# Performance work log

Measured on AMD Instinct MI355X. Metric: run time of the kernel, lower is better.

## Reference

```python
import jax, jax.numpy as jnp
import numpy as np

SDIM, EDIM, HID, DEPTH = 128, 128, 64, 4
CUTOFF, EPS = 5.0, 1e-6
N, E = 40000, 512000
MSG_IN = 2 * SDIM + EDIM + 2   # [s_src, s_dst, e, dist, ea_d]
SCAL_IN = SDIM + HID


def silu(x):
    return x * jax.nn.sigmoid(x)


def setup_inputs() -> dict:
    key = jax.random.key(0)
    ks = jax.random.split(key, 16)

    def w(k, shape, fan):
        return jax.random.normal(k, shape, jnp.float32) / np.float32(np.sqrt(fan))

    return {
        "s": jax.random.normal(ks[0], (N, SDIM), jnp.float32),
        "v": jax.random.normal(ks[1], (N, 3), jnp.float32),
        "e": jax.random.normal(ks[2], (E, EDIM), jnp.float32),
        "edge_index": jax.random.randint(ks[3], (2, E), 0, N),
        "ea_d": jax.random.uniform(ks[4], (E, 1), dtype=jnp.float32),
        "ea_r": jax.random.normal(ks[5], (E, 3), jnp.float32),
        "batch": jnp.zeros((N,), jnp.int32),
        "We1": w(ks[6], (DEPTH, MSG_IN, HID), MSG_IN),
        "be1": jnp.zeros((DEPTH, HID), jnp.float32),
        "We2": w(ks[7], (DEPTH, HID, HID), HID),
        "be2": jnp.zeros((DEPTH, HID), jnp.float32),
        "Weo": w(ks[8], (DEPTH, HID, EDIM), HID),
        "beo": jnp.zeros((DEPTH, EDIM), jnp.float32),
        "Wv": w(ks[9], (DEPTH, HID, 1), HID),
        "bv": jnp.zeros((DEPTH, 1), jnp.float32),
        "Ws1": w(ks[10], (DEPTH, SCAL_IN, HID), SCAL_IN),
        "bs1": jnp.zeros((DEPTH, HID), jnp.float32),
        "Ws2": w(ks[11], (DEPTH, HID, SDIM), HID),
        "bs2": jnp.zeros((DEPTH, SDIM), jnp.float32),
    }


def egnn_forward(s, v, e, src, dst, ea_d,
                 We1, be1, We2, be2, Weo, beo, Wv, bv, Ws1, bs1, Ws2, bs2):
    n = s.shape[0]
    ne = e.shape[0]
    # mean aggregation: per-destination degree (clamped to 1)
    deg = jax.ops.segment_sum(jnp.ones((ne, 1), s.dtype), dst, num_segments=n)
    deg = jnp.maximum(deg, 1.0)
    for i in range(DEPTH):
        rel = v[src] - v[dst]                                          # [E,3]
        dist = jnp.sqrt(jnp.sum(rel * rel, axis=-1, keepdims=True) + EPS)  # [E,1]
        cw = 0.5 * (jnp.cos(jnp.pi * dist / CUTOFF) + 1.0) * (dist < CUTOFF)
        h = jnp.concatenate([s[src], s[dst], e, dist, ea_d], axis=-1)  # [E,MSG_IN]
        m = silu(silu(h @ We1[i] + be1[i]) @ We2[i] + be2[i]) * cw      # [E,HID]
        e = e + m @ Weo[i] + beo[i]                                    # edge residual
        wv = m @ Wv[i] + bv[i]                                         # [E,1]
        v = v + jax.ops.segment_sum(rel * wv, dst, num_segments=n) / deg
        agg = jax.ops.segment_sum(m, dst, num_segments=n) / deg        # [N,HID]
        s = s + silu(jnp.concatenate([s, agg], axis=-1) @ Ws1[i] + bs1[i]) @ Ws2[i] + bs2[i]
    return s, v, e


def reference(s, v, e, edge_index, ea_d, ea_r, batch,
              We1, be1, We2, be2, Weo, beo, Wv, bv, Ws1, bs1, Ws2, bs2):
    del batch, ea_r  # unused in the enhanced (EGCL_Edge_Fast) path
    src, dst = edge_index[0], edge_index[1]
    return egnn_forward(s, v, e, src, dst, ea_d,
                        We1, be1, We2, be2, Weo, beo, Wv, bv, Ws1, bs1, Ws2, bs2)
```

## Files before the change

### kernel.cpp

```cpp
#include <hip/hip_runtime.h>
#include <math.h>

#define N_NODES 40000
#define N_EDGES 512000
#define SDIM 128
#define EDIM 128
#define HID 64
#define DEPTH 4
#define MSG_IN 386
#define SCAL_IN 192
#define CUTOFF 5.0f
#define EPS_D 1e-6f

#define TILE_M 16
#define EW 8
#define ETHREADS 512
#define EBLOCKS 256
#define TWAVES (EBLOCKS * EW)
#define NTILES (N_EDGES / TILE_M)
#define ATILES (N_NODES / TILE_M)
#define SCAN_B 1024
#define SCAN_NB ((N_NODES + SCAN_B - 1) / SCAN_B)

typedef __attribute__((ext_vector_type(8))) short short8;
typedef __attribute__((ext_vector_type(4))) float f32x4;
typedef unsigned long long ull;

__device__ __forceinline__ float silu_f(float x) { return x / (1.0f + __expf(-x)); }

__device__ __forceinline__ unsigned short f2b(float x) {
  union { __bf16 b; unsigned short u; } v;
  v.b = (__bf16)x;
  return v.u;
}

__device__ __forceinline__ float b2f(unsigned short u) {
  union { unsigned int u32; float f; } v; v.u32 = (unsigned int)u << 16; return v.f;
}

__device__ __forceinline__ short8 pack8(f32x4 lo, f32x4 hi) {
  union { unsigned short u[8]; short8 s; } pk;
  pk.u[0] = f2b(lo[0]); pk.u[1] = f2b(lo[1]); pk.u[2] = f2b(lo[2]); pk.u[3] = f2b(lo[3]);
  pk.u[4] = f2b(hi[0]); pk.u[5] = f2b(hi[1]); pk.u[6] = f2b(hi[2]); pk.u[7] = f2b(hi[3]);
  return pk.s;
}

__global__ __launch_bounds__(256) void k_zero(float* __restrict__ p, int n) {
  int i = blockIdx.x * 256 + threadIdx.x;
  int stride = gridDim.x * 256;
  for (; i < n; i += stride) p[i] = 0.0f;
}

__global__ __launch_bounds__(256) void k_cnt(const int* __restrict__ dst,
                                             int* __restrict__ cnt, int ne) {
  int i = blockIdx.x * 256 + threadIdx.x;
  if (i < ne) atomicAdd(&cnt[dst[i]], 1);
}

__global__ __launch_bounds__(256) void k_deginv_cnt(const int* __restrict__ cnt,
                                                    float* __restrict__ deginv, int n) {
  int i = blockIdx.x * 256 + threadIdx.x;
  if (i < n) deginv[i] = 1.0f / fmaxf((float)cnt[i], 1.0f);
}

__global__ __launch_bounds__(256) void k_scan1(const int* __restrict__ cnt,
                                               int* __restrict__ bstart,
                                               int* __restrict__ bsum, int n) {
  __shared__ int tmp[SCAN_B];
  const int base = blockIdx.x * SCAN_B;
  const int tid = threadIdx.x;
  for (int i = tid; i < SCAN_B; i += 256)
    tmp[i] = (base + i < n) ? cnt[base + i] : 0;
  __syncthreads();
  for (int off = 1; off < SCAN_B; off <<= 1) {
    int vals[4];
#pragma unroll
    for (int j = 0; j < 4; ++j) {
      const int i = tid + j * 256;
      vals[j] = (i >= off) ? tmp[i - off] : 0;
    }
    __syncthreads();
#pragma unroll
    for (int j = 0; j < 4; ++j) tmp[tid + j * 256] += vals[j];
    __syncthreads();
  }
  for (int i = tid; i < SCAN_B; i += 256)
    if (base + i < n) bstart[base + i] = tmp[i] - cnt[base + i];
  if (tid == 0) bsum[blockIdx.x] = tmp[SCAN_B - 1];
}

__global__ void k_scan2(int* __restrict__ bsum, int nb) {
  if (threadIdx.x == 0) {
    int run = 0;
    for (int i = 0; i < nb; ++i) { const int v = bsum[i]; bsum[i] = run; run += v; }
  }
}

__global__ __launch_bounds__(256) void k_scan3(int* __restrict__ bstart,
                                               const int* __restrict__ bsum,
                                               int* __restrict__ cursor, int n) {
  int i = blockIdx.x * 256 + threadIdx.x;
  if (i < n) {
    const int v = bstart[i] + bsum[i >> 10];
    bstart[i] = v;
    cursor[i] = v;
  }
}

__global__ __launch_bounds__(256) void k_scatter(const int* __restrict__ srcs,
                                                 const int* __restrict__ dsts,
                                                 const float* __restrict__ ead,
                                                 int* __restrict__ cursor,
                                                 int4* __restrict__ meta, int ne) {
  int i = blockIdx.x * 256 + threadIdx.x;
  if (i < ne) {
    const int d = dsts[i];
    const int pos = atomicAdd(&cursor[d], 1);
    int4 m;
    m.x = i; m.y = srcs[i]; m.z = d; m.w = __float_as_int(ead[i]);
    meta[pos] = m;
  }
}

__global__ __launch_bounds__(256) void k_prep(const int4* __restrict__ meta,
                                              const float* __restrict__ vbuf,
                                              float4* __restrict__ dynA,
                                              float* __restrict__ dynB, int ne) {
  int i = blockIdx.x * 256 + threadIdx.x;
  if (i < ne) {
    const int4 m = meta[i];
    const float dx = vbuf[m.y * 3 + 0] - vbuf[m.z * 3 + 0];
    const float dy = vbuf[m.y * 3 + 1] - vbuf[m.z * 3 + 1];
    const float dz = vbuf[m.y * 3 + 2] - vbuf[m.z * 3 + 2];
    const float dist = sqrtf(dx * dx + dy * dy + dz * dz + EPS_D);
    const float cwv = (dist < CUTOFF)
                          ? 0.5f * (__cosf((float)M_PI / CUTOFF * dist) + 1.0f)
                          : 0.0f;
    dynA[i] = make_float4(dx, dy, dz, dist);
    dynB[i] = cwv;
  }
}

__global__ __launch_bounds__(512, 2) void k_nodeA(
    const float* __restrict__ s, const float* __restrict__ W1,
    const float* __restrict__ be1_,
    unsigned short* __restrict__ SaP, unsigned short* __restrict__ SbP) {
  __shared__ __align__(16) unsigned short W1abt[64 * 264];
  __shared__ __align__(16) unsigned short snS[EW][16 * 136];
  const int tid = threadIdx.x, lane = tid & 63, w = tid >> 6;
  const int c = lane & 15, g = lane >> 4;
  for (int idx = tid; idx < 256 * 64; idx += 512) {
    const int k = idx >> 6, n = idx & 63;
    W1abt[n * 264 + k] = f2b(W1[idx]);
  }
  __syncthreads();
  float be1_l[4];
#pragma unroll
  for (int nt = 0; nt < 4; ++nt) be1_l[nt] = be1_[nt * 16 + c];
  unsigned short* sn = snS[w];

  for (int t = blockIdx.x * EW + w; t < ATILES; t += gridDim.x * EW) {
    const int n0 = t * TILE_M;
    const f32x4* sbase = (const f32x4*)(s + (size_t)n0 * SDIM);
#pragma unroll
    for (int i = 0; i < 4; ++i) {
      const int f = i * 128 + lane * 2;
      const f32x4 a = sbase[f], b = sbase[f + 1];
      *(short8*)&sn[(i * 4 + g) * 136 + c * 8] = pack8(a, b);
    }
    f32x4 aA[4], aB[4];
#pragma unroll
    for (int nt = 0; nt < 4; ++nt) {
      aA[nt] = f32x4{be1_l[nt], be1_l[nt], be1_l[nt], be1_l[nt]};
      aB[nt] = f32x4{0.f, 0.f, 0.f, 0.f};
    }
#pragma unroll
    for (int kc = 0; kc < 4; ++kc) {
      const short8 af = *(const short8*)&sn[c * 136 + kc * 32 + g * 8];
#pragma unroll
      for (int nt = 0; nt < 4; ++nt) {
        const short8 bfA = *(const short8*)&W1abt[(nt * 16 + c) * 264 + kc * 32 + g * 8];
        const short8 bfB = *(const short8*)&W1abt[(nt * 16 + c) * 264 + 128 + kc * 32 + g * 8];
        aA[nt] = __builtin_amdgcn_mfma_f32_16x16x32_bf16(af, bfA, aA[nt], 0, 0, 0);
        aB[nt] = __builtin_amdgcn_mfma_f32_16x16x32_bf16(af, bfB, aB[nt], 0, 0, 0);
      }
    }
#pragma unroll
    for (int r = 0; r < 4; ++r) {
      const size_t row = (size_t)(n0 + g * 4 + r);
      const ull pa = (ull)f2b(aA[0][r]) | ((ull)f2b(aA[1][r]) << 16)
                   | ((ull)f2b(aA[2][r]) << 32) | ((ull)f2b(aA[3][r]) << 48);
      const ull pb = (ull)f2b(aB[0][r]) | ((ull)f2b(aB[1][r]) << 16)
                   | ((ull)f2b(aB[2][r]) << 32) | ((ull)f2b(aB[3][r]) << 48);
      *(ull*)&SaP[row * 64 + c * 4] = pa;
      *(ull*)&SbP[row * 64 + c * 4] = pb;
    }
  }
}

__global__ __launch_bounds__(512, 2) void k_nodeC(
    const float* __restrict__ scur, float* __restrict__ s_dst,
    const float* __restrict__ vcur, float* __restrict__ v_dst,
    float* __restrict__ v_acc, float* __restrict__ agg,
    const float* __restrict__ deginv,
    const float* __restrict__ Ws1_, const float* __restrict__ bs1_,
    const float* __restrict__ Ws2_, const float* __restrict__ bs2_,
    const float* __restrict__ W1n, const float* __restrict__ be1n,
    unsigned short* __restrict__ SaP, unsigned short* __restrict__ SbP,
    int doA) {
  __shared__ __align__(16) unsigned short Ws1t[64 * 200];
  __shared__ __align__(16) unsigned short Ws2t[128 * 72];
  __shared__ __align__(16) unsigned short W1abt[64 * 264];
  __shared__ __align__(16) unsigned short sAS[EW][16 * 200];
  __shared__ __align__(16) unsigned short hS[EW][16 * 72];
  __shared__ float dS[EW][16];
  const int tid = threadIdx.x, lane = tid & 63, w = tid >> 6;
  const int c = lane & 15, g = lane >> 4;
  for (int idx = tid; idx < 192 * 64; idx += 512) {
    const int k = idx >> 6, n = idx & 63;
    Ws1t[n * 200 + k] = f2b(Ws1_[idx]);
  }
  for (int idx = tid; idx < 64 * 128; idx += 512) {
    const int k = idx >> 7, n = idx & 127;
    Ws2t[n * 72 + k] = f2b(Ws2_[idx]);
  }
  if (doA) {
    for (int idx = tid; idx < 256 * 64; idx += 512) {
      const int k = idx >> 6, n = idx & 63;
      W1abt[n * 264 + k] = f2b(W1n[idx]);
    }
  }
  __syncthreads();
  float bs1_l[4], bs2_l[8], be1_l[4];
#pragma unroll
  for (int nt = 0; nt < 4; ++nt) bs1_l[nt] = bs1_[nt * 16 + c];
#pragma unroll
  for (int j = 0; j < 8; ++j) bs2_l[j] = bs2_[j * 16 + c];
#pragma unroll
  for (int nt = 0; nt < 4; ++nt) be1_l[nt] = doA ? be1n[nt * 16 + c] : 0.0f;
  unsigned short* sA = sAS[w];
  unsigned short* hw = hS[w];

  for (int t = blockIdx.x * EW + w; t < ATILES; t += gridDim.x * EW) {
    const int n0 = t * TILE_M;
    if (lane < 16) dS[w][lane] = deginv[n0 + lane];
    if (lane < 48) {
      const int i3 = n0 * 3 + lane;
      v_dst[i3] = vcur[i3] + v_acc[i3] * dS[w][lane / 3];
      v_acc[i3] = 0.0f;
    }
    const f32x4* sbase = (const f32x4*)(scur + (size_t)n0 * SDIM);
#pragma unroll
    for (int i = 0; i < 4; ++i) {
      const int f = i * 128 + lane * 2;
      const f32x4 a = sbase[f], b = sbase[f + 1];
      *(short8*)&sA[(i * 4 + g) * 200 + c * 8] = pack8(a, b);
    }
#pragma unroll
    for (int i = 0; i < 4; ++i) {
      const int row = i * 4 + g;
      float* ab = agg + (size_t)(n0 + row) * HID + c * 4;
      const f32x4 av = *(const f32x4*)ab;
      const float di = dS[w][row];
      union { unsigned short u[4]; ull ll; } pk4;
      pk4.u[0] = f2b(av[0] * di); pk4.u[1] = f2b(av[1] * di);
      pk4.u[2] = f2b(av[2] * di); pk4.u[3] = f2b(av[3] * di);
      *(ull*)&sA[row * 200 + 128 + c * 4] = pk4.ll;
      *(f32x4*)ab = f32x4{0.f, 0.f, 0.f, 0.f};
    }
    f32x4 acc[4];
#pragma unroll
    for (int nt = 0; nt < 4; ++nt)
      acc[nt] = f32x4{bs1_l[nt], bs1_l[nt], bs1_l[nt], bs1_l[nt]};
#pragma unroll
    for (int kc = 0; kc < 6; ++kc) {
      const short8 af = *(const short8*)&sA[c * 200 + kc * 32 + g * 8];
#pragma unroll
      for (int nt = 0; nt < 4; ++nt) {
        const short8 bf = *(const short8*)&Ws1t[(nt * 16 + c) * 200 + kc * 32 + g * 8];
        acc[nt] = __builtin_amdgcn_mfma_f32_16x16x32_bf16(af, bf, acc[nt], 0, 0, 0);
      }
    }
#pragma unroll
    for (int nt = 0; nt < 4; ++nt)
#pragma unroll
      for (int r = 0; r < 4; ++r)
        hw[(g * 4 + r) * 72 + nt * 16 + c] = f2b(silu_f(acc[nt][r]));
    f32x4 o[8];
#pragma unroll
    for (int nt = 0; nt < 8; ++nt) o[nt] = f32x4{0.f, 0.f, 0.f, 0.f};
#pragma unroll
    for (int kc = 0; kc < 2; ++kc) {
      const short8 am = *(const short8*)&hw[c * 72 + kc * 32 + g * 8];
#pragma unroll
      for (int nt = 0; nt < 8; ++nt) {
        const short8 bf = *(const short8*)&Ws2t[(nt * 16 + c) * 72 + kc * 32 + g * 8];
        o[nt] = __builtin_amdgcn_mfma_f32_16x16x32_bf16(am, bf, o[nt], 0, 0, 0);
      }
    }
#pragma unroll
    for (int j = 0; j < 8; ++j) {
      const int col = j * 16 + c;
#pragma unroll
      for (int r = 0; r < 4; ++r) {
        const int row = g * 4 + r;
        const size_t gi = (size_t)(n0 + row) * SDIM + col;
        const float sum = o[j][r] + bs2_l[j] + scur[gi];
        s_dst[gi] = sum;
        if (doA) sA[row * 200 + col] = f2b(sum);
      }
    }
    if (doA) {
      f32x4 aA[4], aB[4];
#pragma unroll
      for (int nt = 0; nt < 4; ++nt) {
        aA[nt] = f32x4{be1_l[nt], be1_l[nt], be1_l[nt], be1_l[nt]};
        aB[nt] = f32x4{0.f, 0.f, 0.f, 0.f};
      }
#pragma unroll
      for (int kc = 0; kc < 4; ++kc) {
        const short8 af = *(const short8*)&sA[c * 200 + kc * 32 + g * 8];
#pragma unroll
        for (int nt = 0; nt < 4; ++nt) {
          const short8 bfA = *(const short8*)&W1abt[(nt * 16 + c) * 264 + kc * 32 + g * 8];
          const short8 bfB = *(const short8*)&W1abt[(nt * 16 + c) * 264 + 128 + kc * 32 + g * 8];
          aA[nt] = __builtin_amdgcn_mfma_f32_16x16x32_bf16(af, bfA, aA[nt], 0, 0, 0);
          aB[nt] = __builtin_amdgcn_mfma_f32_16x16x32_bf16(af, bfB, aB[nt], 0, 0, 0);
        }
      }
#pragma unroll
      for (int r = 0; r < 4; ++r) {
        const size_t row = (size_t)(n0 + g * 4 + r);
        const ull pa = (ull)f2b(aA[0][r]) | ((ull)f2b(aA[1][r]) << 16)
                     | ((ull)f2b(aA[2][r]) << 32) | ((ull)f2b(aA[3][r]) << 48);
        const ull pb = (ull)f2b(aB[0][r]) | ((ull)f2b(aB[1][r]) << 16)
                     | ((ull)f2b(aB[2][r]) << 32) | ((ull)f2b(aB[3][r]) << 48);
        *(ull*)&SaP[row * 64 + c * 4] = pa;
        *(ull*)&SbP[row * 64 + c * 4] = pb;
      }
    }
  }
}

template <typename TI, typename TO>
__global__ __launch_bounds__(ETHREADS, 1) void k_edge_mfma(
    const TI* __restrict__ e_src, TO* __restrict__ e_dst,
    const unsigned short* __restrict__ SaP, const unsigned short* __restrict__ SbP,
    const int4* __restrict__ meta, const float4* __restrict__ dynA,
    const float* __restrict__ dynB,
    const float* __restrict__ W1e,
    const float* __restrict__ w1d, const float* __restrict__ w1a,
    const float* __restrict__ We2_, const float* __restrict__ be2_,
    const float* __restrict__ Weo_, const float* __restrict__ beo_,
    const float* __restrict__ Wv_, const float* __restrict__ bv_,
    float* __restrict__ v_acc, float* __restrict__ agg) {
  constexpr bool IN16 = (sizeof(TI) == 2);
  constexpr bool OUT16 = (sizeof(TO) == 2);
  __shared__ __align__(16) unsigned short W1t[64 * 136];
  __shared__ __align__(16) unsigned short We2t[64 * 72];
  __shared__ __align__(16) unsigned short WeoT[128 * 72];
  __shared__ __align__(16) unsigned short eT[EW][TILE_M * 136];
  __shared__ __align__(16) float hm[EW][TILE_M * 68];
  __shared__ __align__(16) float sbufS[EW][2][160];

  const int tid = threadIdx.x;
  const int lane = tid & 63;
  const int w = tid >> 6;
  const int c = lane & 15;
  const int g = lane >> 4;

  for (int idx = tid; idx < 128 * 64; idx += ETHREADS) {
    const int k = idx >> 6, n = idx & 63;
    W1t[n * 136 + k] = f2b(W1e[idx]);
  }
  for (int idx = tid; idx < 64 * 64; idx += ETHREADS) {
    const int k = idx >> 6, n = idx & 63;
    We2t[n * 72 + k] = f2b(We2_[idx]);
  }
  for (int idx = tid; idx < 64 * 128; idx += ETHREADS) {
    const int k = idx >> 7, n = idx & 127;
    WeoT[n * 72 + k] = f2b(Weo_[idx]);
  }
  __syncthreads();

  float w1d_l[4], w1a_l[4], be2_l[4], Wv_l[4], beo_l[8];
#pragma unroll
  for (int nt = 0; nt < 4; ++nt) {
    w1d_l[nt] = w1d[nt * 16 + c];
    w1a_l[nt] = w1a[nt * 16 + c];
    be2_l[nt] = be2_[nt * 16 + c];
    Wv_l[nt]  = Wv_[nt * 16 + c];
  }
#pragma unroll
  for (int nt = 0; nt < 8; ++nt) beo_l[nt] = beo_[nt * 16 + c];
  const float bv0 = bv_[0];

  unsigned short* eTw = eT[w];
  float* hmw = hm[w];

  f32x4 eAf[8];
  short8 eAb[4];
  ull sabA[4], sabB[4];
  int4 metaR = {0, 0, 0, 0};
  float4 dynAR = {0.f, 0.f, 0.f, 0.f};
  float cwR = 0.f;

  const int t0 = blockIdx.x * EW + w;
  int cur = 0;

  {
    float* sb0 = &sbufS[w][0][0];
    int* sbi0 = (int*)sb0;
    if (lane < 16) {
      const int pos = t0 * TILE_M + lane;
      const int4 m = meta[pos];
      const float4 da = dynA[pos];
      const float cwv = dynB[pos];
      sb0[lane] = da.w; sb0[16 + lane] = cwv; sb0[32 + lane] = __int_as_float(m.w);
      sb0[48 + lane] = da.x; sb0[64 + lane] = da.y; sb0[80 + lane] = da.z;
      sbi0[96 + lane] = m.y; sbi0[112 + lane] = m.z; sbi0[128 + lane] = m.x;
    }
    if constexpr (IN16) {
      const int erc = sbi0[128 + c];
      const TI* rowp = e_src + (size_t)erc * EDIM;
#pragma unroll
      for (int kc = 0; kc < 4; ++kc)
        eAb[kc] = *(const short8*)(rowp + kc * 32 + g * 8);
    } else {
#pragma unroll
      for (int i = 0; i < 4; ++i) {
        const int er = sbi0[128 + i * 4 + g];
        const f32x4* eb = (const f32x4*)(e_src + (size_t)er * EDIM);
        eAf[i * 2] = eb[c * 2];
        eAf[i * 2 + 1] = eb[c * 2 + 1];
      }
    }
#pragma unroll
    for (int r = 0; r < 4; ++r) {
      sabA[r] = *(const ull*)&SaP[(size_t)sbi0[96 + g * 4 + r] * 64 + c * 4];
      sabB[r] = *(const ull*)&SbP[(size_t)sbi0[112 + g * 4 + r] * 64 + c * 4];
    }
    if (t0 + TWAVES < NTILES && lane < 16) {
      const int pos = (t0 + TWAVES) * TILE_M + lane;
      metaR = meta[pos]; dynAR = dynA[pos]; cwR = dynB[pos];
    }
  }

  for (int t = t0; t < NTILES; t += TWAVES) {
    const bool hasNext = (t + TWAVES) < NTILES;
    float* sbC = &sbufS[w][cur][0];
    int* sbiC = (int*)sbC;
    float* sbN = &sbufS[w][cur ^ 1][0];
    int* sbiN = (int*)sbN;

    if (hasNext && lane < 16) {
      sbN[lane] = dynAR.w; sbN[16 + lane] = cwR; sbN[32 + lane] = __int_as_float(metaR.w);
      sbN[48 + lane] = dynAR.x; sbN[64 + lane] = dynAR.y; sbN[80 + lane] = dynAR.z;
      sbiN[96 + lane] = metaR.y; sbiN[112 + lane] = metaR.z; sbiN[128 + lane] = metaR.x;
    }

    short8 afT[4];
    if constexpr (IN16) {
#pragma unroll
      for (int kc = 0; kc < 4; ++kc) afT[kc] = eAb[kc];
    } else {
#pragma unroll
      for (int i = 0; i < 4; ++i)
        *(short8*)&eT[w][(i * 4 + g) * 136 + c * 8] = pack8(eAf[i * 2], eAf[i * 2 + 1]);
    }

    float dist_r[4], cw_r[4], ea_r[4];
#pragma unroll
    for (int r = 0; r < 4; ++r) {
      const int row = g * 4 + r;
      dist_r[r] = sbC[row]; cw_r[r] = sbC[16 + row]; ea_r[r] = sbC[32 + row];
    }
    f32x4 acc[4];
#pragma unroll
    for (int nt = 0; nt < 4; ++nt)
#pragma unroll
      for (int r = 0; r < 4; ++r)
        acc[nt][r] = b2f((unsigned short)(sabA[r] >> (nt * 16)))
                   + b2f((unsigned short)(sabB[r] >> (nt * 16)))
                   + dist_r[r] * w1d_l[nt] + ea_r[r] * w1a_l[nt];

    if (hasNext) {
      if constexpr (IN16) {
        const int erc = sbiN[128 + c];
        const TI* rowp = e_src + (size_t)erc * EDIM;
#pragma unroll
        for (int kc = 0; kc < 4; ++kc)
          eAb[kc] = *(const short8*)(rowp + kc * 32 + g * 8);
      } else {
#pragma unroll
        for (int i = 0; i < 4; ++i) {
          const int er = sbiN[128 + i * 4 + g];
          const f32x4* eb = (const f32x4*)(e_src + (size_t)er * EDIM);
          eAf[i * 2] = eb[c * 2];
          eAf[i * 2 + 1] = eb[c * 2 + 1];
        }
      }
#pragma unroll
      for (int r = 0; r < 4; ++r) {
        sabA[r] = *(const ull*)&SaP[(size_t)sbiN[96 + g * 4 + r] * 64 + c * 4];
        sabB[r] = *(const ull*)&SbP[(size_t)sbiN[112 + g * 4 + r] * 64 + c * 4];
      }
      if (t + 2 * TWAVES < NTILES && lane < 16) {
        const int pos = (t + 2 * TWAVES) * TILE_M + lane;
        metaR = meta[pos]; dynAR = dynA[pos]; cwR = dynB[pos];
      }
    }

#pragma unroll
    for (int kc = 0; kc < 4; ++kc) {
      short8 af;
      if constexpr (IN16)
        af = afT[kc];
      else
        af = *(const short8*)&eTw[c * 136 + kc * 32 + g * 8];
#pragma unroll
      for (int nt = 0; nt < 4; ++nt) {
        const short8 bf = *(const short8*)&W1t[(nt * 16 + c) * 136 + kc * 32 + g * 8];
        acc[nt] = __builtin_amdgcn_mfma_f32_16x16x32_bf16(af, bf, acc[nt], 0, 0, 0);
      }
    }
#pragma unroll
    for (int nt = 0; nt < 4; ++nt)
#pragma unroll
      for (int r = 0; r < 4; ++r)
        hmw[(g * 4 + r) * 68 + nt * 16 + c] = silu_f(acc[nt][r]);

    f32x4 acc2[4];
#pragma unroll
    for (int nt = 0; nt < 4; ++nt)
      acc2[nt] = f32x4{be2_l[nt], be2_l[nt], be2_l[nt], be2_l[nt]};
#pragma unroll
    for (int kc = 0; kc < 2; ++kc) {
      const f32x4 lo = *(const f32x4*)&hmw[c * 68 + kc * 32 + g * 8];
      const f32x4 hi = *(const f32x4*)&hmw[c * 68 + kc * 32 + g * 8 + 4];
      const short8 am = pack8(lo, hi);
#pragma unroll
      for (int nt = 0; nt < 4; ++nt) {
        const short8 bf = *(const short8*)&We2t[(nt * 16 + c) * 72 + kc * 32 + g * 8];
        acc2[nt] = __builtin_amdgcn_mfma_f32_16x16x32_bf16(am, bf, acc2[nt], 0, 0, 0);
      }
    }
    float mval[4][4];
#pragma unroll
    for (int nt = 0; nt < 4; ++nt)
#pragma unroll
      for (int r = 0; r < 4; ++r)
        mval[nt][r] = silu_f(acc2[nt][r]) * cw_r[r];

#pragma unroll
    for (int nt = 0; nt < 4; ++nt)
#pragma unroll
      for (int r = 0; r < 4; ++r)
        hmw[(g * 4 + r) * 68 + nt * 16 + c] = mval[nt][r];

#pragma unroll
    for (int r = 0; r < 4; ++r) {
      float s = mval[0][r] * Wv_l[0];
#pragma unroll
      for (int nt = 1; nt < 4; ++nt) s = fmaf(mval[nt][r], Wv_l[nt], s);
      s += __shfl_xor(s, 1); s += __shfl_xor(s, 2);
      s += __shfl_xor(s, 4); s += __shfl_xor(s, 8);
      if (c == 0) sbC[144 + g * 4 + r] = s + bv0;
    }

    {
      float accum = 0.f;
#pragma unroll
      for (int row = 0; row < 16; ++row) {
        accum += hmw[row * 68 + lane];
        const int dd = sbiC[112 + row];
        const bool cut = (row == 15) || (sbiC[113 + row] != dd);
        if (cut) {
          atomicAdd(&agg[(size_t)dd * HID + lane], accum);
          accum = 0.f;
        }
      }
    }
    if (lane < 3) {
      float accum = 0.f;
#pragma unroll
      for (int row = 0; row < 16; ++row) {
        accum = fmaf(sbC[48 + 16 * lane + row], sbC[144 + row], accum);
        const int dd = sbiC[112 + row];
        const bool cut = (row == 15) || (sbiC[113 + row] != dd);
        if (cut) {
          atomicAdd(&v_acc[(size_t)dd * 3 + lane], accum);
          accum = 0.f;
        }
      }
    }

    f32x4 oacc[8];
#pragma unroll
    for (int nt = 0; nt < 8; ++nt)
      oacc[nt] = f32x4{beo_l[nt], beo_l[nt], beo_l[nt], beo_l[nt]};
#pragma unroll
    for (int kc = 0; kc < 2; ++kc) {
      const f32x4 lo = *(const f32x4*)&hmw[c * 68 + kc * 32 + g * 8];
      const f32x4 hi = *(const f32x4*)&hmw[c * 68 + kc * 32 + g * 8 + 4];
      const short8 am = pack8(lo, hi);
#pragma unroll
      for (int nt = 0; nt < 8; ++nt) {
        const short8 bf = *(const short8*)&WeoT[(nt * 16 + c) * 72 + kc * 32 + g * 8];
        oacc[nt] = __builtin_amdgcn_mfma_f32_16x16x32_bf16(am, bf, oacc[nt], 0, 0, 0);
      }
    }

#pragma unroll
    for (int h2 = 0; h2 < 2; ++h2) {
#pragma unroll
      for (int nt = 0; nt < 4; ++nt)
#pragma unroll
        for (int r = 0; r < 4; ++r)
          hmw[(g * 4 + r) * 68 + nt * 16 + c] = oacc[h2 * 4 + nt][r];
#pragma unroll
      for (int q = 0; q < 4; ++q) {
        const int row = q * 4 + g;
        const int er = sbiC[128 + row];
        const f32x4 val = *(const f32x4*)&hmw[row * 68 + c * 4];
        f32x4 old;
        if constexpr (IN16) {
          const ull ov = *(const ull*)&e_src[(size_t)er * EDIM + h2 * 64 + c * 4];
#pragma unroll
          for (int j = 0; j < 4; ++j)
            old[j] = b2f((unsigned short)(ov >> (16 * j)));
        } else {
          old = *(const f32x4*)&e_src[(size_t)er * EDIM + h2 * 64 + c * 4];
        }
        const f32x4 sum = val + old;
        if constexpr (OUT16) {
          union { unsigned short u[4]; ull ll; } pk4;
          pk4.u[0] = f2b(sum[0]); pk4.u[1] = f2b(sum[1]);
          pk4.u[2] = f2b(sum[2]); pk4.u[3] = f2b(sum[3]);
          *(ull*)&e_dst[(size_t)er * EDIM + h2 * 64 + c * 4] = pk4.ll;
        } else {
          *(f32x4*)&e_dst[(size_t)er * EDIM + h2 * 64 + c * 4] = sum;
        }
      }
    }
    cur ^= 1;
  }
}

extern "C" void kernel_launch(void* const* d_in, const int* in_sizes, int n_in,
                              void* d_out, int out_size, void* d_ws, size_t ws_size,
                              hipStream_t stream) {
  const float* s_in = (const float*)d_in[0];
  const float* v_in = (const float*)d_in[1];
  const float* e_in = (const float*)d_in[2];
  const int*   eidx = (const int*)d_in[3];
  const float* ead  = (const float*)d_in[4];
  const float* We1 = (const float*)d_in[7];
  const float* be1 = (const float*)d_in[8];
  const float* We2 = (const float*)d_in[9];
  const float* be2 = (const float*)d_in[10];
  const float* Weo = (const float*)d_in[11];
  const float* beo = (const float*)d_in[12];
  const float* Wv  = (const float*)d_in[13];
  const float* bv  = (const float*)d_in[14];
  const float* Ws1 = (const float*)d_in[15];
  const float* bs1 = (const float*)d_in[16];
  const float* Ws2 = (const float*)d_in[17];
  const float* bs2 = (const float*)d_in[18];

  float* out_s = (float*)d_out;
  float* out_v = out_s + (size_t)N_NODES * SDIM;
  float* out_e = out_v + (size_t)N_NODES * 3;

  float* ws     = (float*)d_ws;
  float* deginv = ws;
  float* v_acc  = deginv + N_NODES;
  float* agg    = v_acc + (size_t)3 * N_NODES;
  unsigned short* SaP = (unsigned short*)(agg + (size_t)64 * N_NODES);
  unsigned short* SbP = SaP + (size_t)64 * N_NODES;
  int* cnt     = (int*)(SbP + (size_t)64 * N_NODES);
  int* bstart  = cnt + N_NODES;
  int* cursor  = bstart + N_NODES;
  int* bsum    = cursor + N_NODES;
  int4* meta   = (int4*)(bsum + 64);
  float4* dynA = (float4*)(meta + N_EDGES);
  float* dynB  = (float*)(dynA + N_EDGES);
  unsigned short* eb16 = (unsigned short*)(dynB + N_EDGES);

  const size_t NEED = (size_t)((char*)(eb16 + (size_t)N_EDGES * EDIM) - (char*)d_ws);
  const bool u16e = (ws_size >= NEED);

  const int* srcs = eidx;
  const int* dsts = eidx + N_EDGES;

  hipLaunchKernelGGL(k_zero, dim3(512), dim3(256), 0, stream,
                     deginv, (1 + 3 + 64) * N_NODES);
  hipLaunchKernelGGL(k_zero, dim3(64), dim3(256), 0, stream,
                     (float*)cnt, N_NODES);
  hipLaunchKernelGGL(k_cnt, dim3((N_EDGES + 255) / 256), dim3(256), 0, stream,
                     dsts, cnt, N_EDGES);
  hipLaunchKernelGGL(k_deginv_cnt, dim3((N_NODES + 255) / 256), dim3(256), 0, stream,
                     cnt, deginv, N_NODES);
  hipLaunchKernelGGL(k_scan1, dim3(SCAN_NB), dim3(256), 0, stream,
                     cnt, bstart, bsum, N_NODES);
  hipLaunchKernelGGL(k_scan2, dim3(1), dim3(64), 0, stream, bsum, SCAN_NB);
  hipLaunchKernelGGL(k_scan3, dim3((N_NODES + 255) / 256), dim3(256), 0, stream,
                     bstart, bsum, cursor, N_NODES);
  hipLaunchKernelGGL(k_scatter, dim3((N_EDGES + 255) / 256), dim3(256), 0, stream,
                     srcs, dsts, ead, cursor, meta, N_EDGES);

  hipLaunchKernelGGL(k_nodeA, dim3(512), dim3(512), 0, stream,
                     s_in, We1, be1, SaP, SbP);

  for (int i = 0; i < DEPTH; ++i) {
    const float* W1i = We1 + (size_t)i * MSG_IN * HID;
    const int dn = (i + 1 < DEPTH) ? i + 1 : i;
    hipLaunchKernelGGL(k_prep, dim3((N_EDGES + 255) / 256), dim3(256), 0, stream,
                       meta, (i == 0) ? v_in : out_v, dynA, dynB, N_EDGES);
#define EDGE_ARGS                                                              \
      SaP, SbP, meta, dynA, dynB,                                              \
      W1i + 256 * HID, W1i + 384 * HID, W1i + 385 * HID,                       \
      We2 + (size_t)i * HID * HID, be2 + i * HID,                              \
      Weo + (size_t)i * HID * EDIM, beo + i * EDIM,                            \
      Wv + i * HID, bv + i, v_acc, agg
    if (u16e) {
      if (i == 0)
        k_edge_mfma<float, unsigned short>
            <<<dim3(EBLOCKS), dim3(ETHREADS), 0, stream>>>(e_in, eb16, EDGE_ARGS);
      else if (i == DEPTH - 1)
        k_edge_mfma<unsigned short, float>
            <<<dim3(EBLOCKS), dim3(ETHREADS), 0, stream>>>(eb16, out_e, EDGE_ARGS);
      else
        k_edge_mfma<unsigned short, unsigned short>
            <<<dim3(EBLOCKS), dim3(ETHREADS), 0, stream>>>(eb16, eb16, EDGE_ARGS);
    } else {
      k_edge_mfma<float, float>
          <<<dim3(EBLOCKS), dim3(ETHREADS), 0, stream>>>(
              (i == 0) ? e_in : out_e, out_e, EDGE_ARGS);
    }
#undef EDGE_ARGS
    hipLaunchKernelGGL(k_nodeC, dim3(EBLOCKS), dim3(512), 0, stream,
                       (i == 0) ? s_in : out_s, out_s,
                       (i == 0) ? v_in : out_v, out_v,
                       v_acc, agg, deginv,
                       Ws1 + (size_t)i * SCAL_IN * HID, bs1 + i * HID,
                       Ws2 + (size_t)i * HID * SDIM, bs2 + i * SDIM,
                       We1 + (size_t)dn * MSG_IN * HID, be1 + dn * HID,
                       SaP, SbP, (i + 1 < DEPTH) ? 1 : 0);
  }
}
```

Baseline: 762.1 us.

## Add slim bf16-input edge kernel with smaller LDS for two blocks per CU

Splits the edge kernel into a fp32-input 'big' variant (used for layer 0) and a new bf16-input 'slim' variant used for the remaining layers. The slim kernel drops the per-wave eT staging buffer and the float hm scratch, replacing them with a bf16 hidden buffer that is reused for the output transpose. This shrinks LDS and registers enough to request two blocks per CU and to launch twice as many blocks. The output write is reorganised so each lane stores contiguous 4-wide chunks per 16-column slice. The risks are higher register pressure under the tighter launch bounds and extra LDS round trips in the output path.

```diff
diff --git a/kernel.cpp b/kernel.cpp
--- a/kernel.cpp
+++ b/kernel.cpp
@@ -15,8 +15,8 @@
 #define TILE_M 16
 #define EW 8
 #define ETHREADS 512
-#define EBLOCKS 256
-#define TWAVES (EBLOCKS * EW)
+#define EBLK_BIG 256
+#define EBLK_SLIM 512
 #define NTILES (N_EDGES / TILE_M)
 #define ATILES (N_NODES / TILE_M)
 #define SCAN_B 1024
@@ -342,9 +342,9 @@
   }
 }
 
-template <typename TI, typename TO>
-__global__ __launch_bounds__(ETHREADS, 1) void k_edge_mfma(
-    const TI* __restrict__ e_src, TO* __restrict__ e_dst,
+template <typename TO>
+__global__ __launch_bounds__(ETHREADS, 1) void k_edge_big(
+    const float* __restrict__ e_src, TO* __restrict__ e_dst,
     const unsigned short* __restrict__ SaP, const unsigned short* __restrict__ SbP,
     const int4* __restrict__ meta, const float4* __restrict__ dynA,
     const float* __restrict__ dynB,
@@ -354,7 +354,6 @@
     const float* __restrict__ Weo_, const float* __restrict__ beo_,
     const float* __restrict__ Wv_, const float* __restrict__ bv_,
     float* __restrict__ v_acc, float* __restrict__ agg) {
-  constexpr bool IN16 = (sizeof(TI) == 2);
   constexpr bool OUT16 = (sizeof(TO) == 2);
   __shared__ __align__(16) unsigned short W1t[64 * 136];
   __shared__ __align__(16) unsigned short We2t[64 * 72];
@@ -399,7 +398,6 @@
   float* hmw = hm[w];
 
   f32x4 eAf[8];
-  short8 eAb[4];
   ull sabA[4], sabB[4];
   int4 metaR = {0, 0, 0, 0};
   float4 dynAR = {0.f, 0.f, 0.f, 0.f};
@@ -420,34 +418,26 @@
       sb0[48 + lane] = da.x; sb0[64 + lane] = da.y; sb0[80 + lane] = da.z;
       sbi0[96 + lane] = m.y; sbi0[112 + lane] = m.z; sbi0[128 + lane] = m.x;
     }
-    if constexpr (IN16) {
-      const int erc = sbi0[128 + c];
-      const TI* rowp = e_src + (size_t)erc * EDIM;
-#pragma unroll
-      for (int kc = 0; kc < 4; ++kc)
-        eAb[kc] = *(const short8*)(rowp + kc * 32 + g * 8);
-    } else {
-#pragma unroll
-      for (int i = 0; i < 4; ++i) {
-        const int er = sbi0[128 + i * 4 + g];
-        const f32x4* eb = (const f32x4*)(e_src + (size_t)er * EDIM);
-        eAf[i * 2] = eb[c * 2];
-        eAf[i * 2 + 1] = eb[c * 2 + 1];
-      }
+#pragma unroll
+    for (int i = 0; i < 4; ++i) {
+      const int er = sbi0[128 + i * 4 + g];
+      const f32x4* eb = (const f32x4*)(e_src + (size_t)er * EDIM);
+      eAf[i * 2] = eb[c * 2];
+      eAf[i * 2 + 1] = eb[c * 2 + 1];
     }
 #pragma unroll
     for (int r = 0; r < 4; ++r) {
       sabA[r] = *(const ull*)&SaP[(size_t)sbi0[96 + g * 4 + r] * 64 + c * 4];
       sabB[r] = *(const ull*)&SbP[(size_t)sbi0[112 + g * 4 + r] * 64 + c * 4];
     }
-    if (t0 + TWAVES < NTILES && lane < 16) {
-      const int pos = (t0 + TWAVES) * TILE_M + lane;
+    if (t0 + EBLK_BIG * EW < NTILES && lane < 16) {
+      const int pos = (t0 + EBLK_BIG * EW) * TILE_M + lane;
       metaR = meta[pos]; dynAR = dynA[pos]; cwR = dynB[pos];
     }
   }
 
-  for (int t = t0; t < NTILES; t += TWAVES) {
-    const bool hasNext = (t + TWAVES) < NTILES;
+  for (int t = t0; t < NTILES; t += EBLK_BIG * EW) {
+    const bool hasNext = (t + EBLK_BIG * EW) < NTILES;
     float* sbC = &sbufS[w][cur][0];
     int* sbiC = (int*)sbC;
     float* sbN = &sbufS[w][cur ^ 1][0];
@@ -459,15 +449,9 @@
       sbiN[96 + lane] = metaR.y; sbiN[112 + lane] = metaR.z; sbiN[128 + lane] = metaR.x;
     }
 
-    short8 afT[4];
-    if constexpr (IN16) {
-#pragma unroll
-      for (int kc = 0; kc < 4; ++kc) afT[kc] = eAb[kc];
-    } else {
-#pragma unroll
-      for (int i = 0; i < 4; ++i)
-        *(short8*)&eT[w][(i * 4 + g) * 136 + c * 8] = pack8(eAf[i * 2], eAf[i * 2 + 1]);
-    }
+#pragma unroll
+    for (int i = 0; i < 4; ++i)
+      *(short8*)&eTw[(i * 4 + g) * 136 + c * 8] = pack8(eAf[i * 2], eAf[i * 2 + 1]);
 
     float dist_r[4], cw_r[4], ea_r[4];
 #pragma unroll
@@ -485,39 +469,27 @@
                    + dist_r[r] * w1d_l[nt] + ea_r[r] * w1a_l[nt];
 
     if (hasNext) {
-      if constexpr (IN16) {
-        const int erc = sbiN[128 + c];
-        const TI* rowp = e_src + (size_t)erc * EDIM;
-#pragma unroll
-        for (int kc = 0; kc < 4; ++kc)
-          eAb[kc] = *(const short8*)(rowp + kc * 32 + g * 8);
-      } else {
-#pragma unroll
-        for (int i = 0; i < 4; ++i) {
-          const int er = sbiN[128 + i * 4 + g];
-          const f32x4* eb = (const f32x4*)(e_src + (size_t)er * EDIM);
-          eAf[i * 2] = eb[c * 2];
-          eAf[i * 2 + 1] = eb[c * 2 + 1];
-        }
+#pragma unroll
+      for (int i = 0; i < 4; ++i) {
+        const int er = sbiN[128 + i * 4 + g];
+        const f32x4* eb = (const f32x4*)(e_src + (size_t)er * EDIM);
+        eAf[i * 2] = eb[c * 2];
+        eAf[i * 2 + 1] = eb[c * 2 + 1];
       }
 #pragma unroll
       for (int r = 0; r < 4; ++r) {
         sabA[r] = *(const ull*)&SaP[(size_t)sbiN[96 + g * 4 + r] * 64 + c * 4];
         sabB[r] = *(const ull*)&SbP[(size_t)sbiN[112 + g * 4 + r] * 64 + c * 4];
       }
-      if (t + 2 * TWAVES < NTILES && lane < 16) {
-        const int pos = (t + 2 * TWAVES) * TILE_M + lane;
+      if (t + 2 * EBLK_BIG * EW < NTILES && lane < 16) {
+        const int pos = (t + 2 * EBLK_BIG * EW) * TILE_M + lane;
         metaR = meta[pos]; dynAR = dynA[pos]; cwR = dynB[pos];
       }
     }
 
 #pragma unroll
     for (int kc = 0; kc < 4; ++kc) {
-      short8 af;
-      if constexpr (IN16)
-        af = afT[kc];
-      else
-        af = *(const short8*)&eTw[c * 136 + kc * 32 + g * 8];
+      const short8 af = *(const short8*)&eTw[c * 136 + kc * 32 + g * 8];
 #pragma unroll
       for (int nt = 0; nt < 4; ++nt) {
         const short8 bf = *(const short8*)&W1t[(nt * 16 + c) * 136 + kc * 32 + g * 8];
@@ -623,15 +595,7 @@
         const int row = q * 4 + g;
         const int er = sbiC[128 + row];
         const f32x4 val = *(const f32x4*)&hmw[row * 68 + c * 4];
-        f32x4 old;
-        if constexpr (IN16) {
-          const ull ov = *(const ull*)&e_src[(size_t)er * EDIM + h2 * 64 + c * 4];
-#pragma unroll
-          for (int j = 0; j < 4; ++j)
-            old[j] = b2f((unsigned short)(ov >> (16 * j)));
-        } else {
-          old = *(const f32x4*)&e_src[(size_t)er * EDIM + h2 * 64 + c * 4];
-        }
+        const f32x4 old = *(const f32x4*)&e_src[(size_t)er * EDIM + h2 * 64 + c * 4];
         const f32x4 sum = val + old;
         if constexpr (OUT16) {
           union { unsigned short u[4]; ull ll; } pk4;
@@ -639,7 +603,274 @@
           pk4.u[2] = f2b(sum[2]); pk4.u[3] = f2b(sum[3]);
           *(ull*)&e_dst[(size_t)er * EDIM + h2 * 64 + c * 4] = pk4.ll;
         } else {
-          *(f32x4*)&e_dst[(size_t)er * EDIM + h2 * 64 + c * 4] = sum;
+          *(f32x4*)&((float*)e_dst)[(size_t)er * EDIM + h2 * 64 + c * 4] = sum;
+        }
+      }
+    }
+    cur ^= 1;
+  }
+}
+
+template <typename TO>
+__global__ __launch_bounds__(ETHREADS, 2) void k_edge_slim(
+    const unsigned short* __restrict__ e_src, TO* __restrict__ e_dst,
+    const unsigned short* __restrict__ SaP, const unsigned short* __restrict__ SbP,
+    const int4* __restrict__ meta, const float4* __restrict__ dynA,
+    const float* __restrict__ dynB,
+    const float* __restrict__ W1e,
+    const float* __restrict__ w1d, const float* __restrict__ w1a,
+    const float* __restrict__ We2_, const float* __restrict__ be2_,
+    const float* __restrict__ Weo_, const float* __restrict__ beo_,
+    const float* __restrict__ Wv_, const float* __restrict__ bv_,
+    float* __restrict__ v_acc, float* __restrict__ agg) {
+  constexpr bool OUT16 = (sizeof(TO) == 2);
+  __shared__ __align__(16) unsigned short W1t[64 * 136];
+  __shared__ __align__(16) unsigned short We2t[64 * 72];
+  __shared__ __align__(16) unsigned short WeoT[128 * 72];
+  __shared__ __align__(16) unsigned short hmB[EW][16 * 72];
+  __shared__ __align__(16) float sbufS[EW][2][160];
+
+  const int tid = threadIdx.x;
+  const int lane = tid & 63;
+  const int w = tid >> 6;
+  const int c = lane & 15;
+  const int g = lane >> 4;
+
+  for (int idx = tid; idx < 128 * 64; idx += ETHREADS) {
+    const int k = idx >> 6, n = idx & 63;
+    W1t[n * 136 + k] = f2b(W1e[idx]);
+  }
+  for (int idx = tid; idx < 64 * 64; idx += ETHREADS) {
+    const int k = idx >> 6, n = idx & 63;
+    We2t[n * 72 + k] = f2b(We2_[idx]);
+  }
+  for (int idx = tid; idx < 64 * 128; idx += ETHREADS) {
+    const int k = idx >> 7, n = idx & 127;
+    WeoT[n * 72 + k] = f2b(Weo_[idx]);
+  }
+  __syncthreads();
+
+  float w1d_l[4], w1a_l[4], be2_l[4], Wv_l[4], beo_l[8];
+#pragma unroll
+  for (int nt = 0; nt < 4; ++nt) {
+    w1d_l[nt] = w1d[nt * 16 + c];
+    w1a_l[nt] = w1a[nt * 16 + c];
+    be2_l[nt] = be2_[nt * 16 + c];
+    Wv_l[nt]  = Wv_[nt * 16 + c];
+  }
+#pragma unroll
+  for (int nt = 0; nt < 8; ++nt) beo_l[nt] = beo_[nt * 16 + c];
+  const float bv0 = bv_[0];
+
+  unsigned short* hbw = hmB[w];
+
+  short8 eAb[4];
+  ull sabA[4], sabB[4];
+  int4 metaR = {0, 0, 0, 0};
+  float4 dynAR = {0.f, 0.f, 0.f, 0.f};
+  float cwR = 0.f;
+
+  const int t0 = blockIdx.x * EW + w;
+  int cur = 0;
+
+  if (t0 < NTILES) {
+    float* sb0 = &sbufS[w][0][0];
+    int* sbi0 = (int*)sb0;
+    if (lane < 16) {
+      const int pos = t0 * TILE_M + lane;
+      const int4 m = meta[pos];
+      const float4 da = dynA[pos];
+      const float cwv = dynB[pos];
+      sb0[lane] = da.w; sb0[16 + lane] = cwv; sb0[32 + lane] = __int_as_float(m.w);
+      sb0[48 + lane] = da.x; sb0[64 + lane] = da.y; sb0[80 + lane] = da.z;
+      sbi0[96 + lane] = m.y; sbi0[112 + lane] = m.z; sbi0[128 + lane] = m.x;
+    }
+    {
+      const int erc = sbi0[128 + c];
+      const unsigned short* rowp = e_src + (size_t)erc * EDIM;
+#pragma unroll
+      for (int kc = 0; kc < 4; ++kc)
+        eAb[kc] = *(const short8*)(rowp + kc * 32 + g * 8);
+    }
+#pragma unroll
+    for (int r = 0; r < 4; ++r) {
+      sabA[r] = *(const ull*)&SaP[(size_t)sbi0[96 + g * 4 + r] * 64 + c * 4];
+      sabB[r] = *(const ull*)&SbP[(size_t)sbi0[112 + g * 4 + r] * 64 + c * 4];
+    }
+    if (t0 + EBLK_SLIM * EW < NTILES && lane < 16) {
+      const int pos = (t0 + EBLK_SLIM * EW) * TILE_M + lane;
+      metaR = meta[pos]; dynAR = dynA[pos]; cwR = dynB[pos];
+    }
+  }
+
+  for (int t = t0; t < NTILES; t += EBLK_SLIM * EW) {
+    const bool hasNext = (t + EBLK_SLIM * EW) < NTILES;
+    float* sbC = &sbufS[w][cur][0];
+    int* sbiC = (int*)sbC;
+    float* sbN = &sbufS[w][cur ^ 1][0];
+    int* sbiN = (int*)sbN;
+
+    if (hasNext && lane < 16) {
+      sbN[lane] = dynAR.w; sbN[16 + lane] = cwR; sbN[32 + lane] = __int_as_float(metaR.w);
+      sbN[48 + lane] = dynAR.x; sbN[64 + lane] = dynAR.y; sbN[80 + lane] = dynAR.z;
+      sbiN[96 + lane] = metaR.y; sbiN[112 + lane] = metaR.z; sbiN[128 + lane] = metaR.x;
+    }
+
+    float dist_r[4], cw_r[4], ea_r[4];
+#pragma unroll
+    for (int r = 0; r < 4; ++r) {
+      const int row = g * 4 + r;
+      dist_r[r] = sbC[row]; cw_r[r] = sbC[16 + row]; ea_r[r] = sbC[32 + row];
+    }
+    f32x4 acc[4];
+#pragma unroll
+    for (int nt = 0; nt < 4; ++nt)
+#pragma unroll
+      for (int r = 0; r < 4; ++r)
+        acc[nt][r] = b2f((unsigned short)(sabA[r] >> (nt * 16)))
+                   + b2f((unsigned short)(sabB[r] >> (nt * 16)))
+                   + dist_r[r] * w1d_l[nt] + ea_r[r] * w1a_l[nt];
+
+#pragma unroll
+    for (int kc = 0; kc < 4; ++kc) {
+      const short8 af = eAb[kc];
+#pragma unroll
+      for (int nt = 0; nt < 4; ++nt) {
+        const short8 bf = *(const short8*)&W1t[(nt * 16 + c) * 136 + kc * 32 + g * 8];
+        acc[nt] = __builtin_amdgcn_mfma_f32_16x16x32_bf16(af, bf, acc[nt], 0, 0, 0);
+      }
+    }
+
+    if (hasNext) {
+      {
+        const int erc = sbiN[128 + c];
+        const unsigned short* rowp = e_src + (size_t)erc * EDIM;
+#pragma unroll
+        for (int kc = 0; kc < 4; ++kc)
+          eAb[kc] = *(const short8*)(rowp + kc * 32 + g * 8);
+      }
+#pragma unroll
+      for (int r = 0; r < 4; ++r) {
+        sabA[r] = *(const ull*)&SaP[(size_t)sbiN[96 + g * 4 + r] * 64 + c * 4];
+        sabB[r] = *(const ull*)&SbP[(size_t)sbiN[112 + g * 4 + r] * 64 + c * 4];
+      }
+      if (t + 2 * EBLK_SLIM * EW < NTILES && lane < 16) {
+        const int pos = (t + 2 * EBLK_SLIM * EW) * TILE_M + lane;
+        metaR = meta[pos]; dynAR = dynA[pos]; cwR = dynB[pos];
+      }
+    }
+
+#pragma unroll
+    for (int nt = 0; nt < 4; ++nt)
+#pragma unroll
+      for (int r = 0; r < 4; ++r)
+        hbw[(g * 4 + r) * 72 + nt * 16 + c] = f2b(silu_f(acc[nt][r]));
+
+    f32x4 acc2[4];
+#pragma unroll
+    for (int nt = 0; nt < 4; ++nt)
+      acc2[nt] = f32x4{be2_l[nt], be2_l[nt], be2_l[nt], be2_l[nt]};
+#pragma unroll
+    for (int kc = 0; kc < 2; ++kc) {
+      const short8 am = *(const short8*)&hbw[c * 72 + kc * 32 + g * 8];
+#pragma unroll
+      for (int nt = 0; nt < 4; ++nt) {
+        const short8 bf = *(const short8*)&We2t[(nt * 16 + c) * 72 + kc * 32 + g * 8];
+        acc2[nt] = __builtin_amdgcn_mfma_f32_16x16x32_bf16(am, bf, acc2[nt], 0, 0, 0);
+      }
+    }
+    float mval[4][4];
+#pragma unroll
+    for (int nt = 0; nt < 4; ++nt)
+#pragma unroll
+      for (int r = 0; r < 4; ++r)
+        mval[nt][r] = silu_f(acc2[nt][r]) * cw_r[r];
+
+#pragma unroll
+    for (int nt = 0; nt < 4; ++nt)
+#pragma unroll
+      for (int r = 0; r < 4; ++r)
+        hbw[(g * 4 + r) * 72 + nt * 16 + c] = f2b(mval[nt][r]);
+
+#pragma unroll
+    for (int r = 0; r < 4; ++r) {
+      float s = mval[0][r] * Wv_l[0];
+#pragma unroll
+      for (int nt = 1; nt < 4; ++nt) s = fmaf(mval[nt][r], Wv_l[nt], s);
+      s += __shfl_xor(s, 1); s += __shfl_xor(s, 2);
+      s += __shfl_xor(s, 4); s += __shfl_xor(s, 8);
+      if (c == 0) sbC[144 + g * 4 + r] = s + bv0;
+    }
+
+#pragma unroll
+    for (int nt = 0; nt < 4; ++nt) {
+      float accum = 0.f;
+#pragma unroll
+      for (int r = 0; r < 4; ++r) {
+        accum += mval[nt][r];
+        const int row = g * 4 + r;
+        const int dd = sbiC[112 + row];
+        const bool cut = (r == 3) || (sbiC[113 + row] != dd);
+        if (cut) {
+          atomicAdd(&agg[(size_t)dd * HID + nt * 16 + c], accum);
+          accum = 0.f;
+        }
+      }
+    }
+    if (lane < 3) {
+      float accum = 0.f;
+#pragma unroll
+      for (int row = 0; row < 16; ++row) {
+        accum = fmaf(sbC[48 + 16 * lane + row], sbC[144 + row], accum);
+        const int dd = sbiC[112 + row];
+        const bool cut = (row == 15) || (sbiC[113 + row] != dd);
+        if (cut) {
+          atomicAdd(&v_acc[(size_t)dd * 3 + lane], accum);
+          accum = 0.f;
+        }
+      }
+    }
+
+    f32x4 oacc[8];
+#pragma unroll
+    for (int nt = 0; nt < 8; ++nt)
+      oacc[nt] = f32x4{beo_l[nt], beo_l[nt], beo_l[nt], beo_l[nt]};
+#pragma unroll
+    for (int kc = 0; kc < 2; ++kc) {
+      const short8 am = *(const short8*)&hbw[c * 72 + kc * 32 + g * 8];
+#pragma unroll
+      for (int nt = 0; nt < 8; ++nt) {
+        const short8 bf = *(const short8*)&WeoT[(nt * 16 + c) * 72 + kc * 32 + g * 8];
+        oacc[nt] = __builtin_amdgcn_mfma_f32_16x16x32_bf16(am, bf, oacc[nt], 0, 0, 0);
+      }
+    }
+
+    {
+      float* bq = (float*)hbw;
+      const int row2 = lane >> 2, cq = lane & 3;
+      const int er2 = sbiC[128 + row2];
+#pragma unroll
+      for (int nt = 0; nt < 8; ++nt) {
+#pragma unroll
+        for (int r = 0; r < 4; ++r)
+          bq[(g * 4 + r) * 18 + c] = oacc[nt][r];
+        const float v0 = bq[row2 * 18 + cq * 4 + 0];
+        const float v1 = bq[row2 * 18 + cq * 4 + 1];
+        const float v2 = bq[row2 * 18 + cq * 4 + 2];
+        const float v3 = bq[row2 * 18 + cq * 4 + 3];
+        const size_t gi = (size_t)er2 * EDIM + nt * 16 + cq * 4;
+        const ull ov = *(const ull*)&e_src[gi];
+        const float s0 = v0 + b2f((unsigned short)(ov));
+        const float s1 = v1 + b2f((unsigned short)(ov >> 16));
+        const float s2 = v2 + b2f((unsigned short)(ov >> 32));
+        const float s3 = v3 + b2f((unsigned short)(ov >> 48));
+        if constexpr (OUT16) {
+          union { unsigned short u[4]; ull ll; } pk4;
+          pk4.u[0] = f2b(s0); pk4.u[1] = f2b(s1);
+          pk4.u[2] = f2b(s2); pk4.u[3] = f2b(s3);
+          *(ull*)&e_dst[gi] = pk4.ll;
+        } else {
+          *(f32x4*)&((float*)e_dst)[gi] = f32x4{s0, s1, s2, s3};
         }
       }
     }
@@ -725,21 +956,21 @@
       Wv + i * HID, bv + i, v_acc, agg
     if (u16e) {
       if (i == 0)
-        k_edge_mfma<float, unsigned short>
-            <<<dim3(EBLOCKS), dim3(ETHREADS), 0, stream>>>(e_in, eb16, EDGE_ARGS);
+        k_edge_big<unsigned short>
+            <<<dim3(EBLK_BIG), dim3(ETHREADS), 0, stream>>>(e_in, eb16, EDGE_ARGS);
       else if (i == DEPTH - 1)
-        k_edge_mfma<unsigned short, float>
-            <<<dim3(EBLOCKS), dim3(ETHREADS), 0, stream>>>(eb16, out_e, EDGE_ARGS);
+        k_edge_slim<float>
+            <<<dim3(EBLK_SLIM), dim3(ETHREADS), 0, stream>>>(eb16, out_e, EDGE_ARGS);
       else
-        k_edge_mfma<unsigned short, unsigned short>
-            <<<dim3(EBLOCKS), dim3(ETHREADS), 0, stream>>>(eb16, eb16, EDGE_ARGS);
+        k_edge_slim<unsigned short>
+            <<<dim3(EBLK_SLIM), dim3(ETHREADS), 0, stream>>>(eb16, eb16, EDGE_ARGS);
     } else {
-      k_edge_mfma<float, float>
-          <<<dim3(EBLOCKS), dim3(ETHREADS), 0, stream>>>(
+      k_edge_big<float>
+          <<<dim3(EBLK_BIG), dim3(ETHREADS), 0, stream>>>(
               (i == 0) ? e_in : out_e, out_e, EDGE_ARGS);
     }
 #undef EDGE_ARGS
-    hipLaunchKernelGGL(k_nodeC, dim3(EBLOCKS), dim3(512), 0, stream,
+    hipLaunchKernelGGL(k_nodeC, dim3(256), dim3(512), 0, stream,
                        (i == 0) ? s_in : out_s, out_s,
                        (i == 0) ? v_in : out_v, out_v,
                        v_acc, agg, deginv,
```

Result: slower. 820.6 us (+7.7%).
